# Optimization experiments

Hardware: AMD Instinct MI355X
Metric: run time of the kernel (lower is better)

## Reference

```python
import jax, jax.numpy as jnp
import numpy as np

EPS = 1e-5
GROUPS = 8

def group_norm(x, gamma, beta):
    # x: [B,C,H,W], 8 groups
    B, C, H, W = x.shape
    xg = x.reshape(B, GROUPS, C // GROUPS, H, W)
    mu = jnp.mean(xg, axis=(2, 3, 4), keepdims=True)
    var = jnp.mean((xg - mu) ** 2, axis=(2, 3, 4), keepdims=True)
    xn = ((xg - mu) * jax.lax.rsqrt(var + EPS)).reshape(B, C, H, W)
    return xn * gamma[None, :, None, None] + beta[None, :, None, None]

def setup_inputs() -> dict:
    key = jax.random.key(0)
    ks = jax.random.split(key, 7)
    B, C, H, W = 4, 256, 64, 64
    x = jax.random.normal(ks[0], (B, C, H, W), dtype=jnp.float32)
    gamma = jnp.ones((C,), dtype=jnp.float32)
    beta = jnp.zeros((C,), dtype=jnp.float32)
    s = 1.0 / np.sqrt(C)
    w_qkv = jax.random.normal(ks[1], (3 * C, C), dtype=jnp.float32) * s
    b_qkv = jnp.zeros((3 * C,), dtype=jnp.float32)
    w_proj = jax.random.normal(ks[2], (C, C), dtype=jnp.float32) * s
    b_proj = jnp.zeros((C,), dtype=jnp.float32)
    return {"x": x, "gamma": gamma, "beta": beta, "w_qkv": w_qkv,
            "b_qkv": b_qkv, "w_proj": w_proj, "b_proj": b_proj}

def reference(x, gamma, beta, w_qkv, b_qkv, w_proj, b_proj):
    B, C, H, W = x.shape
    N = H * W
    h = group_norm(x, gamma, beta)
    # 1x1 conv == per-pixel matmul
    qkv = jnp.einsum('bchw,oc->bohw', h, w_qkv) + b_qkv[None, :, None, None]
    q, k, v = jnp.split(qkv, 3, axis=1)  # each [B,C,H,W]
    q = q.reshape(B, C, N).transpose(0, 2, 1)   # [B,N,C]
    k = k.reshape(B, C, N)                      # [B,C,N]
    v = v.reshape(B, C, N).transpose(0, 2, 1)   # [B,N,C]
    attn = jax.nn.softmax(jnp.einsum('bnc,bcm->bnm', q, k) / jnp.sqrt(jnp.float32(C)), axis=-1)
    out = jnp.einsum('bnm,bmc->bnc', attn, v)   # [B,N,C]
    out = out.transpose(0, 2, 1).reshape(B, C, H, W)
    proj = jnp.einsum('bchw,oc->bohw', out, w_proj) + b_proj[None, :, None, None]
    return x + proj
```

## Files before the change

### kernel.cpp

```cpp
#include <hip/hip_runtime.h>
#include <hip/hip_bf16.h>
#include <math.h>

#define B 4
#define C 256
#define G 8
#define N 4096
#define EPSV 1e-5f
#define SCALE 0.0625f

typedef __attribute__((ext_vector_type(8))) short short8;
typedef __attribute__((ext_vector_type(16))) float f32x16;
typedef unsigned short ushort_t;
typedef unsigned int uint_t;

__device__ __forceinline__ ushort_t f2bf(float f) {
    union { float f; uint_t u; } c; c.f = f;
    uint_t u = c.u;
    uint_t r = (u + 0x7FFFu + ((u >> 16) & 1u)) >> 16;
    return (ushort_t)r;
}
__device__ __forceinline__ float bf2f(ushort_t h) {
    union { uint_t u; float f; } c; c.u = ((uint_t)h) << 16;
    return c.f;
}
__device__ __forceinline__ uint_t pack2(float a, float b) {
    return (uint_t)f2bf(a) | ((uint_t)f2bf(b) << 16);
}
__device__ __forceinline__ uint_t cvtpk_bf16(float lo, float hi) {
    uint_t r;
    asm("v_cvt_pk_bf16_f32 %0, %1, %2" : "=v"(r) : "v"(lo), "v"(hi));
    return r;
}
__device__ __forceinline__ void gl_lds16(const void* g, void* l) {
    __builtin_amdgcn_global_load_lds(
        (const __attribute__((address_space(1))) void*)g,
        (__attribute__((address_space(3))) void*)l, 16, 0, 0);
}

__global__ __launch_bounds__(256) void wconv(const float* __restrict__ wq,
        const float* __restrict__ wp, ushort_t* __restrict__ wbf) {
    int idx = blockIdx.x*256 + threadIdx.x;
    #pragma unroll
    for (int p = 0; p < 4; p++) {
        int id = idx + p*16384;
        float4 v = (id < 49152) ? ((const float4*)wq)[id] : ((const float4*)wp)[id - 49152];
        uint2 pk; pk.x = pack2(v.x, v.y); pk.y = pack2(v.z, v.w);
        *(uint2*)&wbf[(size_t)id*4] = pk;
    }
}

__global__ __launch_bounds__(256) void gn_partial(const float* __restrict__ x,
                                                  float* __restrict__ partials) {
    int blk = blockIdx.x;
    int bg = blk >> 3;
    int part = blk & 7;
    const float4* xp4 = (const float4*)(x + (size_t)bg * (32 * N) + (size_t)part * (32 * N / 8));
    float s = 0.f, ss = 0.f;
    for (int i = threadIdx.x; i < 4096; i += 256) {
        float4 v = xp4[i];
        s  += v.x + v.y + v.z + v.w;
        ss += v.x*v.x + v.y*v.y + v.z*v.z + v.w*v.w;
    }
    __shared__ float rs[256], rss[256];
    rs[threadIdx.x] = s; rss[threadIdx.x] = ss;
    __syncthreads();
    for (int off = 128; off > 0; off >>= 1) {
        if (threadIdx.x < off) {
            rs[threadIdx.x]  += rs[threadIdx.x + off];
            rss[threadIdx.x] += rss[threadIdx.x + off];
        }
        __syncthreads();
    }
    if (threadIdx.x == 0) {
        partials[(bg*8 + part)*2]     = rs[0];
        partials[(bg*8 + part)*2 + 1] = rss[0];
    }
}

__global__ void gn_final(const float* __restrict__ partials, float* __restrict__ stats) {
    int t = threadIdx.x;
    if (t < 32) {
        float s = 0.f, ss = 0.f;
        for (int p = 0; p < 8; p++) {
            s  += partials[(t*8 + p)*2];
            ss += partials[(t*8 + p)*2 + 1];
        }
        const float inv = 1.f / 131072.f;
        float mu = s * inv;
        float var = fmaxf(ss * inv - mu*mu, 0.f);
        stats[t*2]     = mu;
        stats[t*2 + 1] = rsqrtf(var + EPSV);
    }
}

__global__ __launch_bounds__(256) void norm_bf16(const float* __restrict__ x,
        const float* __restrict__ gamma, const float* __restrict__ beta,
        const float* __restrict__ stats, ushort_t* __restrict__ hbf) {
    int b = blockIdx.z, c0 = blockIdx.y*64, n0 = blockIdx.x*64;
    int t = threadIdx.x;
    int cq = t >> 4, nq = t & 15;
    ushort_t hv[4][4];
    #pragma unroll
    for (int i = 0; i < 4; i++) {
        int c = c0 + cq*4 + i;
        int g = c >> 5;
        float mu = stats[(b*G+g)*2], rs = stats[(b*G+g)*2+1];
        float ga = gamma[c]*rs;
        float be = beta[c] - mu*ga;
        float4 v = *(const float4*)&x[((size_t)(b*C + c))*N + n0 + nq*4];
        hv[i][0] = f2bf(v.x*ga + be);
        hv[i][1] = f2bf(v.y*ga + be);
        hv[i][2] = f2bf(v.z*ga + be);
        hv[i][3] = f2bf(v.w*ga + be);
    }
    #pragma unroll
    for (int j = 0; j < 4; j++) {
        uint2 pk;
        pk.x = (uint_t)hv[0][j] | ((uint_t)hv[1][j]<<16);
        pk.y = (uint_t)hv[2][j] | ((uint_t)hv[3][j]<<16);
        *(uint2*)&hbf[((size_t)(b*N + n0 + nq*4 + j))*256 + c0 + cq*4] = pk;
    }
}

__global__ __launch_bounds__(256) void qkv_mfma(const ushort_t* __restrict__ hbf,
        const ushort_t* __restrict__ wbf, const float* __restrict__ bias,
        ushort_t* __restrict__ qbf, ushort_t* __restrict__ kimg, ushort_t* __restrict__ vimg) {
    int b = blockIdx.z, o0 = blockIdx.y*128, n0 = blockIdx.x*128;
    int tid = threadIdx.x;
    int w = tid>>6, l = tid&63, l31 = l&31, lh = l>>5;
    __shared__ short Ws[2][8192];
    __shared__ short Hs[2][8192];

    const ushort_t* wb = wbf + (size_t)o0*256;
    const ushort_t* hb = hbf + ((size_t)b*N + n0)*256;

    auto stage = [&](int bb, int c0) {
        #pragma unroll
        for (int q = 0; q < 4; q++) {
            int u0 = (q*4 + w)*64;
            int u  = u0 + l;
            int row = u & 127, ch = u >> 7;
            gl_lds16(wb + (size_t)row*256 + c0 + ch*8, &Ws[bb][u0*8]);
            gl_lds16(hb + (size_t)row*256 + c0 + ch*8, &Hs[bb][u0*8]);
        }
    };

    f32x16 acc[4];
    #pragma unroll
    for (int nf = 0; nf < 4; nf++)
        #pragma unroll
        for (int r = 0; r < 16; r++) acc[nf][r] = 0.f;

    stage(0, 0);
    __syncthreads();
    for (int t = 0; t < 4; t++) {
        int bb = t & 1;
        if (t < 3) stage(bb^1, (t+1)*64);
        short8 af[4];
        #pragma unroll
        for (int s = 0; s < 4; s++)
            af[s] = *(const short8*)&Ws[bb][((2*s+lh)*128 + w*32 + l31)*8];
        #pragma unroll
        for (int nf = 0; nf < 4; nf++) {
            #pragma unroll
            for (int s = 0; s < 4; s++) {
                short8 hf = *(const short8*)&Hs[bb][((2*s+lh)*128 + nf*32 + l31)*8];
                acc[nf] = __builtin_amdgcn_mfma_f32_32x32x16_bf16(af[s], hf, acc[nf], 0, 0, 0);
            }
        }
        __syncthreads();
    }

    int ow = o0 + w*32;
    float bv[16];
    #pragma unroll
    for (int r = 0; r < 16; r++) bv[r] = bias[ow + (r&3) + 8*(r>>2) + 4*lh];

    if (ow < 256) {
        #pragma unroll
        for (int nf = 0; nf < 4; nf++) {
            int n = n0 + nf*32 + l31;
            ushort_t* row = qbf + ((size_t)(b*N + n))*256 + ow;
            #pragma unroll
            for (int rp = 0; rp < 8; rp++) {
                int r0 = rp*2;
                int cl = (r0&3) + 8*(r0>>2) + 4*lh;
                uint_t wd = cvtpk_bf16((acc[nf][r0]+bv[r0])*SCALE, (acc[nf][r0+1]+bv[r0+1])*SCALE);
                *(uint_t*)(row + cl) = wd;
            }
        }
    } else if (ow < 512) {
        int cb = ow - 256;
        #pragma unroll
        for (int nf = 0; nf < 4; nf++) {
            int n = n0 + nf*32 + l31;
            ushort_t* tbase = kimg + (size_t)b*1048576 + (size_t)(n>>5)*8192
                            + (size_t)l31*8 + 4*lh;
            #pragma unroll
            for (int g = 0; g < 4; g++) {
                uint2 pk;
                pk.x = pack2(acc[nf][g*4+0]+bv[g*4+0], acc[nf][g*4+1]+bv[g*4+1]);
                pk.y = pack2(acc[nf][g*4+2]+bv[g*4+2], acc[nf][g*4+3]+bv[g*4+3]);
                *(uint2*)(tbase + (size_t)((cb>>3)+g)*256) = pk;
            }
        }
    } else {
        int cb = ow - 512;
        #pragma unroll
        for (int nf = 0; nf < 4; nf++) {
            int n = n0 + nf*32 + l31;
            ushort_t* tbase = vimg + (size_t)b*1048576 + (size_t)(n>>5)*8192
                            + (size_t)(l31>>3)*2048 + (l31&7);
            #pragma unroll
            for (int r = 0; r < 16; r++) {
                int cl = (r&3) + 8*(r>>2) + 4*lh;
                tbase[(size_t)(cb+cl)*8] = f2bf(acc[nf][r] + bv[r]);
            }
        }
    }
}

__global__ __launch_bounds__(256, 2) void attn_mfma(const ushort_t* __restrict__ qbf,
        const ushort_t* __restrict__ kimg, const ushort_t* __restrict__ vimg,
        ushort_t* __restrict__ part, float* __restrict__ ml) {
    int f = blockIdx.x;
    int comb = f & 15;
    int qt  = f >> 4;
    int b   = comb >> 2;
    int kvq = comb & 3;
    constexpr int NT = 32;
    int w = threadIdx.x >> 6;
    int l = threadIdx.x & 63;
    int l31 = l & 31, lh = l >> 5;

    __shared__ short KV[2][2][8192];

    int qbase = qt*128 + w*32;
    short8 qf[16];
    {
        const ushort_t* qrow = qbf + ((size_t)(b*N + qbase + l31))*256;
        #pragma unroll
        for (int s = 0; s < 16; s++)
            qf[s] = *(const short8*)(qrow + s*16 + lh*8);
    }

    f32x16 ot[8];
    #pragma unroll
    for (int mc = 0; mc < 8; mc++)
        #pragma unroll
        for (int r = 0; r < 16; r++) ot[mc][r] = 0.f;
    float m = -INFINITY, lsum = 0.f;

    const char* kbase = (const char*)kimg + (size_t)b*2097152;
    const char* vbase = (const char*)vimg + (size_t)b*2097152;

    auto stage = [&](int slot, int t) {
        int tile = kvq*32 + t;
        const char* kt = kbase + (size_t)tile*16384;
        const char* vt = vbase + (size_t)tile*16384;
        #pragma unroll
        for (int q = 0; q < 4; q++) {
            int u0 = (w*4 + q)*64;
            gl_lds16(kt + (u0 + l)*16, &KV[slot][0][u0*8]);
            gl_lds16(vt + (u0 + l)*16, &KV[slot][1][u0*8]);
        }
    };

    stage(0, 0);

    for (int t = 0; t < NT; t++) {
        int slot = t & 1;
        __syncthreads();
        if (t+1 < NT) stage(slot^1, t+1);

        f32x16 st0, st1;
        #pragma unroll
        for (int r = 0; r < 16; r++) { st0[r] = 0.f; st1[r] = 0.f; }
        const short* kb_ = &KV[slot][0][0];
        __builtin_amdgcn_s_setprio(1);
        #pragma unroll
        for (int s = 0; s < 8; s++) {
            short8 ka = *(const short8*)(kb_ + ((size_t)((4*s   + lh)*32 + l31))*8);
            short8 kc = *(const short8*)(kb_ + ((size_t)((4*s+2 + lh)*32 + l31))*8);
            st0 = __builtin_amdgcn_mfma_f32_32x32x16_bf16(ka, qf[2*s],   st0, 0, 0, 0);
            st1 = __builtin_amdgcn_mfma_f32_32x32x16_bf16(kc, qf[2*s+1], st1, 0, 0, 0);
        }
        __builtin_amdgcn_s_setprio(0);

        float sv[16];
        #pragma unroll
        for (int r = 0; r < 16; r++) sv[r] = st0[r] + st1[r];
        float pmax = sv[0];
        #pragma unroll
        for (int r = 1; r < 16; r++) pmax = fmaxf(pmax, sv[r]);
        pmax = fmaxf(pmax, __shfl_xor(pmax, 32));
        if (!__all(pmax <= m + 8.0f)) {
            float mn = fmaxf(m, pmax);
            float fac = __expf(m - mn);
            m = mn;
            lsum *= fac;
            #pragma unroll
            for (int mc = 0; mc < 8; mc++)
                #pragma unroll
                for (int r = 0; r < 16; r++) ot[mc][r] *= fac;
        }
        float p[16]; float ls = 0.f;
        #pragma unroll
        for (int r = 0; r < 16; r++) { p[r] = __expf(sv[r] - m); ls += p[r]; }
        ls += __shfl_xor(ls, 32);
        lsum += ls;

        short8 pf0, pf1;
        {
            uint_t x0 = cvtpk_bf16(p[0], p[1]);
            uint_t y0 = cvtpk_bf16(p[4], p[5]);
            uint_t x1 = cvtpk_bf16(p[2], p[3]);
            uint_t y1 = cvtpk_bf16(p[6], p[7]);
            auto r0 = __builtin_amdgcn_permlane32_swap(x0, y0, false, false);
            auto r1 = __builtin_amdgcn_permlane32_swap(x1, y1, false, false);
            union { uint_t u[4]; short8 s8; } u_;
            u_.u[0] = r0[0]; u_.u[1] = r1[0]; u_.u[2] = r0[1]; u_.u[3] = r1[1];
            pf0 = u_.s8;
            uint_t x2 = cvtpk_bf16(p[8],  p[9]);
            uint_t y2 = cvtpk_bf16(p[12], p[13]);
            uint_t x3 = cvtpk_bf16(p[10], p[11]);
            uint_t y3 = cvtpk_bf16(p[14], p[15]);
            auto r2 = __builtin_amdgcn_permlane32_swap(x2, y2, false, false);
            auto r3 = __builtin_amdgcn_permlane32_swap(x3, y3, false, false);
            union { uint_t u[4]; short8 s8; } u2_;
            u2_.u[0] = r2[0]; u2_.u[1] = r3[0]; u2_.u[2] = r2[1]; u2_.u[3] = r3[1];
            pf1 = u2_.s8;
        }

        const short* vb_ = &KV[slot][1][0];
        __builtin_amdgcn_s_setprio(1);
        #pragma unroll
        for (int mc = 0; mc < 8; mc++) {
            short8 v0 = *(const short8*)(vb_ + ((size_t)((lh)*256   + mc*32 + l31))*8);
            short8 v1 = *(const short8*)(vb_ + ((size_t)((2+lh)*256 + mc*32 + l31))*8);
            ot[mc] = __builtin_amdgcn_mfma_f32_32x32x16_bf16(v0, pf0, ot[mc], 0, 0, 0);
            ot[mc] = __builtin_amdgcn_mfma_f32_32x32x16_bf16(v1, pf1, ot[mc], 0, 0, 0);
        }
        __builtin_amdgcn_s_setprio(0);
    }

    float invl = 1.f / lsum;
    ushort_t* pbase = part + (size_t)kvq*4194304 + ((size_t)(b*N + qbase + l31))*256;
    #pragma unroll
    for (int mc = 0; mc < 8; mc++)
        #pragma unroll
        for (int rp = 0; rp < 8; rp++) {
            int r0 = rp*2;
            uint_t wd = cvtpk_bf16(ot[mc][r0]*invl, ot[mc][r0+1]*invl);
            int c0 = (r0 & 3) + 8*(r0 >> 2) + 4*lh + 32*mc;
            *(uint_t*)(pbase + c0) = wd;
        }
    if (l < 32) {
        size_t row = (size_t)kvq*16384 + b*4096 + qbase + l;
        ml[row*2]     = m;
        ml[row*2 + 1] = lsum;
    }
}

template<int NS>
__global__ __launch_bounds__(256) void attn_merge(const ushort_t* __restrict__ part,
        const float* __restrict__ ml, ushort_t* __restrict__ ob) {
    int t = blockIdx.x*256 + threadIdx.x;
    int row = t >> 5;
    int c8 = (t & 31) * 8;
    float mv[NS], lv[NS];
    float M = -INFINITY;
    #pragma unroll
    for (int i = 0; i < NS; i++) {
        mv[i] = ml[((size_t)i*16384 + row)*2];
        lv[i] = ml[((size_t)i*16384 + row)*2 + 1];
        M = fmaxf(M, mv[i]);
    }
    float wv[NS]; float wsum = 0.f;
    #pragma unroll
    for (int i = 0; i < NS; i++) { wv[i] = __expf(mv[i] - M)*lv[i]; wsum += wv[i]; }
    float inv = 1.f / wsum;
    float o[8];
    #pragma unroll
    for (int e = 0; e < 8; e++) o[e] = 0.f;
    #pragma unroll
    for (int i = 0; i < NS; i++) {
        const ushort_t* p = part + (size_t)i*4194304 + (size_t)row*256 + c8;
        float wi = wv[i]*inv;
        #pragma unroll
        for (int e = 0; e < 8; e++) o[e] += wi*bf2f(p[e]);
    }
    uint4 pk;
    pk.x = pack2(o[0], o[1]);
    pk.y = pack2(o[2], o[3]);
    pk.z = pack2(o[4], o[5]);
    pk.w = pack2(o[6], o[7]);
    *(uint4*)(ob + (size_t)row*256 + c8) = pk;
}

__global__ __launch_bounds__(256) void proj_mfma(const ushort_t* __restrict__ obf,
        const ushort_t* __restrict__ wpbf, const float* __restrict__ bp,
        const float* __restrict__ x, float* __restrict__ out) {
    int b = blockIdx.z, o0 = blockIdx.y*128, n0 = blockIdx.x*128;
    int tid = threadIdx.x;
    int w = tid>>6, l = tid&63, l31 = l&31, lh = l>>5;
    __shared__ short Ws[2][8192];
    __shared__ short Hs[2][8192];

    const ushort_t* wb = wpbf + (size_t)o0*256;
    const ushort_t* hb = obf + ((size_t)b*N + n0)*256;

    auto stage = [&](int bb, int c0) {
        #pragma unroll
        for (int q = 0; q < 4; q++) {
            int u0 = (q*4 + w)*64;
            int u  = u0 + l;
            int row = u & 127, ch = u >> 7;
            gl_lds16(wb + (size_t)row*256 + c0 + ch*8, &Ws[bb][u0*8]);
            gl_lds16(hb + (size_t)row*256 + c0 + ch*8, &Hs[bb][u0*8]);
        }
    };

    f32x16 acc[4];
    #pragma unroll
    for (int nf = 0; nf < 4; nf++)
        #pragma unroll
        for (int r = 0; r < 16; r++) acc[nf][r] = 0.f;

    stage(0, 0);
    __syncthreads();
    for (int t = 0; t < 4; t++) {
        int bb = t & 1;
        if (t < 3) stage(bb^1, (t+1)*64);
        short8 af[4];
        #pragma unroll
        for (int s = 0; s < 4; s++)
            af[s] = *(const short8*)&Ws[bb][((2*s+lh)*128 + w*32 + l31)*8];
        #pragma unroll
        for (int nf = 0; nf < 4; nf++) {
            #pragma unroll
            for (int s = 0; s < 4; s++) {
                short8 hf = *(const short8*)&Hs[bb][((2*s+lh)*128 + nf*32 + l31)*8];
                acc[nf] = __builtin_amdgcn_mfma_f32_32x32x16_bf16(af[s], hf, acc[nf], 0, 0, 0);
            }
        }
        __syncthreads();
    }

    int cw = o0 + w*32;
    float bv[16];
    #pragma unroll
    for (int r = 0; r < 16; r++) bv[r] = bp[cw + (r&3) + 8*(r>>2) + 4*lh];

    #pragma unroll
    for (int nf = 0; nf < 4; nf++) {
        int n = n0 + nf*32 + l31;
        #pragma unroll
        for (int r = 0; r < 16; r++) {
            int cl = (r&3) + 8*(r>>2) + 4*lh;
            size_t a = ((size_t)b*C + cw + cl)*N + n;
            out[a] = acc[nf][r] + bv[r] + x[a];
        }
    }
}

extern "C" void kernel_launch(void* const* d_in, const int* in_sizes, int n_in,
                              void* d_out, int out_size, void* d_ws, size_t ws_size,
                              hipStream_t stream) {
    const float* x      = (const float*)d_in[0];
    const float* gamma  = (const float*)d_in[1];
    const float* beta   = (const float*)d_in[2];
    const float* w_qkv  = (const float*)d_in[3];
    const float* b_qkv  = (const float*)d_in[4];
    const float* w_proj = (const float*)d_in[5];
    const float* b_proj = (const float*)d_in[6];
    float* out = (float*)d_out;
    char* wsb  = (char*)d_ws;

    const size_t MB = 1048576;
    ushort_t* qbf  = (ushort_t*)(wsb);
    ushort_t* kimg = (ushort_t*)(wsb + 8*MB);
    ushort_t* vimg = (ushort_t*)(wsb + 16*MB);
    ushort_t* part = (ushort_t*)(wsb + 24*MB);
    ushort_t* hbf  = part;
    float*    ml   = (float*)  (wsb + 56*MB);
    ushort_t* ob   = (ushort_t*)(wsb + 56*MB + 524288);
    float* partials = (float*) (wsb + 64*MB + 524288);
    float* stats    = partials + 512;
    ushort_t* wbf  = (ushort_t*)(wsb + 64*MB + 524288 + 4096);

    wconv<<<dim3(64), dim3(256), 0, stream>>>(w_qkv, w_proj, wbf);
    gn_partial<<<dim3(256), dim3(256), 0, stream>>>(x, partials);
    gn_final<<<dim3(1), dim3(64), 0, stream>>>(partials, stats);
    norm_bf16<<<dim3(64, 4, 4), dim3(256), 0, stream>>>(x, gamma, beta, stats, hbf);
    qkv_mfma<<<dim3(32, 6, 4), dim3(256), 0, stream>>>(hbf, wbf, b_qkv, qbf, kimg, vimg);
    attn_mfma<<<dim3(512), dim3(256), 0, stream>>>(qbf, kimg, vimg, part, ml);
    attn_merge<4><<<dim3(2048), dim3(256), 0, stream>>>(part, ml, ob);
    proj_mfma<<<dim3(32, 2, 4), dim3(256), 0, stream>>>(ob, wbf + 196608, b_proj, x, out);
}
```

Measured before the change: 151.3 us.

## Fuse groupnorm apply into QKV GEMM, merge weight conversion with stats kernel

The separate norm_bf16 pass is removed. The QKV GEMM now loads fp32 x tiles directly, normalizes them, and writes the bf16 result into shared memory, with the next tile's load overlapping the current MFMAs. Weight conversion and the group-norm partial sums share one launch, and the projection GEMM uses a 64-column N tile to double its grid. This saves a full bf16 round-trip of h and two launches, but each QKV block (6 o-tiles) now re-reads x from global memory, and register pressure grows.

```diff
diff --git a/kernel.cpp b/kernel.cpp
--- a/kernel.cpp
+++ b/kernel.cpp
@@ -38,43 +38,43 @@
         (__attribute__((address_space(3))) void*)l, 16, 0, 0);
 }
 
-__global__ __launch_bounds__(256) void wconv(const float* __restrict__ wq,
+__global__ __launch_bounds__(256) void gn_wconv(const float* __restrict__ x,
+        float* __restrict__ partials, const float* __restrict__ wq,
         const float* __restrict__ wp, ushort_t* __restrict__ wbf) {
-    int idx = blockIdx.x*256 + threadIdx.x;
-    #pragma unroll
-    for (int p = 0; p < 4; p++) {
-        int id = idx + p*16384;
-        float4 v = (id < 49152) ? ((const float4*)wq)[id] : ((const float4*)wp)[id - 49152];
-        uint2 pk; pk.x = pack2(v.x, v.y); pk.y = pack2(v.z, v.w);
-        *(uint2*)&wbf[(size_t)id*4] = pk;
-    }
-}
-
-__global__ __launch_bounds__(256) void gn_partial(const float* __restrict__ x,
-                                                  float* __restrict__ partials) {
     int blk = blockIdx.x;
-    int bg = blk >> 3;
-    int part = blk & 7;
-    const float4* xp4 = (const float4*)(x + (size_t)bg * (32 * N) + (size_t)part * (32 * N / 8));
-    float s = 0.f, ss = 0.f;
-    for (int i = threadIdx.x; i < 4096; i += 256) {
-        float4 v = xp4[i];
-        s  += v.x + v.y + v.z + v.w;
-        ss += v.x*v.x + v.y*v.y + v.z*v.z + v.w*v.w;
-    }
-    __shared__ float rs[256], rss[256];
-    rs[threadIdx.x] = s; rss[threadIdx.x] = ss;
-    __syncthreads();
-    for (int off = 128; off > 0; off >>= 1) {
-        if (threadIdx.x < off) {
-            rs[threadIdx.x]  += rs[threadIdx.x + off];
-            rss[threadIdx.x] += rss[threadIdx.x + off];
-        }
+    if (blk < 256) {
+        int bg = blk >> 3;
+        int part = blk & 7;
+        const float4* xp4 = (const float4*)(x + (size_t)bg * (32 * N) + (size_t)part * (32 * N / 8));
+        float s = 0.f, ss = 0.f;
+        for (int i = threadIdx.x; i < 4096; i += 256) {
+            float4 v = xp4[i];
+            s  += v.x + v.y + v.z + v.w;
+            ss += v.x*v.x + v.y*v.y + v.z*v.z + v.w*v.w;
+        }
+        __shared__ float rs[256], rss[256];
+        rs[threadIdx.x] = s; rss[threadIdx.x] = ss;
         __syncthreads();
-    }
-    if (threadIdx.x == 0) {
-        partials[(bg*8 + part)*2]     = rs[0];
-        partials[(bg*8 + part)*2 + 1] = rss[0];
+        for (int off = 128; off > 0; off >>= 1) {
+            if (threadIdx.x < off) {
+                rs[threadIdx.x]  += rs[threadIdx.x + off];
+                rss[threadIdx.x] += rss[threadIdx.x + off];
+            }
+            __syncthreads();
+        }
+        if (threadIdx.x == 0) {
+            partials[(bg*8 + part)*2]     = rs[0];
+            partials[(bg*8 + part)*2 + 1] = rss[0];
+        }
+    } else {
+        int idx = (blk - 256)*256 + threadIdx.x;
+        #pragma unroll
+        for (int p = 0; p < 4; p++) {
+            int id = idx + p*16384;
+            float4 v = (id < 49152) ? ((const float4*)wq)[id] : ((const float4*)wp)[id - 49152];
+            uint2 pk; pk.x = pack2(v.x, v.y); pk.y = pack2(v.z, v.w);
+            *(uint2*)&wbf[(size_t)id*4] = pk;
+        }
     }
 }
 
@@ -94,57 +94,63 @@
     }
 }
 
-__global__ __launch_bounds__(256) void norm_bf16(const float* __restrict__ x,
-        const float* __restrict__ gamma, const float* __restrict__ beta,
-        const float* __restrict__ stats, ushort_t* __restrict__ hbf) {
-    int b = blockIdx.z, c0 = blockIdx.y*64, n0 = blockIdx.x*64;
-    int t = threadIdx.x;
-    int cq = t >> 4, nq = t & 15;
-    ushort_t hv[4][4];
-    #pragma unroll
-    for (int i = 0; i < 4; i++) {
-        int c = c0 + cq*4 + i;
-        int g = c >> 5;
-        float mu = stats[(b*G+g)*2], rs = stats[(b*G+g)*2+1];
-        float ga = gamma[c]*rs;
-        float be = beta[c] - mu*ga;
-        float4 v = *(const float4*)&x[((size_t)(b*C + c))*N + n0 + nq*4];
-        hv[i][0] = f2bf(v.x*ga + be);
-        hv[i][1] = f2bf(v.y*ga + be);
-        hv[i][2] = f2bf(v.z*ga + be);
-        hv[i][3] = f2bf(v.w*ga + be);
-    }
-    #pragma unroll
-    for (int j = 0; j < 4; j++) {
-        uint2 pk;
-        pk.x = (uint_t)hv[0][j] | ((uint_t)hv[1][j]<<16);
-        pk.y = (uint_t)hv[2][j] | ((uint_t)hv[3][j]<<16);
-        *(uint2*)&hbf[((size_t)(b*N + n0 + nq*4 + j))*256 + c0 + cq*4] = pk;
-    }
-}
-
-__global__ __launch_bounds__(256) void qkv_mfma(const ushort_t* __restrict__ hbf,
-        const ushort_t* __restrict__ wbf, const float* __restrict__ bias,
+__global__ __launch_bounds__(256) void qkv_fused(const float* __restrict__ x,
+        const ushort_t* __restrict__ wbf, const float* __restrict__ gamma,
+        const float* __restrict__ beta, const float* __restrict__ stats,
+        const float* __restrict__ bias,
         ushort_t* __restrict__ qbf, ushort_t* __restrict__ kimg, ushort_t* __restrict__ vimg) {
     int b = blockIdx.z, o0 = blockIdx.y*128, n0 = blockIdx.x*128;
     int tid = threadIdx.x;
     int w = tid>>6, l = tid&63, l31 = l&31, lh = l>>5;
+    int cg = tid >> 5;
+    int nq = tid & 31;
     __shared__ short Ws[2][8192];
     __shared__ short Hs[2][8192];
 
     const ushort_t* wb = wbf + (size_t)o0*256;
-    const ushort_t* hb = hbf + ((size_t)b*N + n0)*256;
-
-    auto stage = [&](int bb, int c0) {
+
+    auto stageW = [&](int bb, int c0) {
         #pragma unroll
         for (int q = 0; q < 4; q++) {
             int u0 = (q*4 + w)*64;
             int u  = u0 + l;
             int row = u & 127, ch = u >> 7;
             gl_lds16(wb + (size_t)row*256 + c0 + ch*8, &Ws[bb][u0*8]);
-            gl_lds16(hb + (size_t)row*256 + c0 + ch*8, &Hs[bb][u0*8]);
         }
     };
+    auto loadX = [&](int c0, float4* xv) {
+        const float* xb = x + ((size_t)b*C + c0 + cg*8)*N + n0 + nq*4;
+        #pragma unroll
+        for (int e = 0; e < 8; e++)
+            xv[e] = *(const float4*)(xb + (size_t)e*N);
+    };
+    auto writeH = [&](int bb, int c0, const float4* xv) {
+        int cbase = c0 + cg*8;
+        int g = cbase >> 5;
+        float mu = stats[(b*G+g)*2], rs = stats[(b*G+g)*2+1];
+        float ga[8], be[8];
+        #pragma unroll
+        for (int e = 0; e < 8; e++) {
+            float gm = gamma[cbase+e];
+            ga[e] = gm*rs;
+            be[e] = beta[cbase+e] - mu*ga[e];
+        }
+        #pragma unroll
+        for (int j = 0; j < 4; j++) {
+            float h[8];
+            #pragma unroll
+            for (int e = 0; e < 8; e++) {
+                float vx = (j==0) ? xv[e].x : (j==1) ? xv[e].y : (j==2) ? xv[e].z : xv[e].w;
+                h[e] = vx*ga[e] + be[e];
+            }
+            uint4 pk;
+            pk.x = pack2(h[0], h[1]);
+            pk.y = pack2(h[2], h[3]);
+            pk.z = pack2(h[4], h[5]);
+            pk.w = pack2(h[6], h[7]);
+            *(uint4*)&Hs[bb][(size_t)(cg*128 + nq*4 + j)*8] = pk;
+        }
+    };
 
     f32x16 acc[4];
     #pragma unroll
@@ -152,11 +158,15 @@
         #pragma unroll
         for (int r = 0; r < 16; r++) acc[nf][r] = 0.f;
 
-    stage(0, 0);
+    float4 xv[8];
+    loadX(0, xv);
+    stageW(0, 0);
+    writeH(0, 0, xv);
     __syncthreads();
+
     for (int t = 0; t < 4; t++) {
         int bb = t & 1;
-        if (t < 3) stage(bb^1, (t+1)*64);
+        if (t < 3) { stageW(bb^1, (t+1)*64); loadX((t+1)*64, xv); }
         short8 af[4];
         #pragma unroll
         for (int s = 0; s < 4; s++)
@@ -169,6 +179,7 @@
                 acc[nf] = __builtin_amdgcn_mfma_f32_32x32x16_bf16(af[s], hf, acc[nf], 0, 0, 0);
             }
         }
+        if (t < 3) writeH(bb^1, (t+1)*64, xv);
         __syncthreads();
     }
 
@@ -402,11 +413,11 @@
 __global__ __launch_bounds__(256) void proj_mfma(const ushort_t* __restrict__ obf,
         const ushort_t* __restrict__ wpbf, const float* __restrict__ bp,
         const float* __restrict__ x, float* __restrict__ out) {
-    int b = blockIdx.z, o0 = blockIdx.y*128, n0 = blockIdx.x*128;
+    int b = blockIdx.z, o0 = blockIdx.y*128, n0 = blockIdx.x*64;
     int tid = threadIdx.x;
     int w = tid>>6, l = tid&63, l31 = l&31, lh = l>>5;
     __shared__ short Ws[2][8192];
-    __shared__ short Hs[2][8192];
+    __shared__ short Hs[2][4096];
 
     const ushort_t* wb = wpbf + (size_t)o0*256;
     const ushort_t* hb = obf + ((size_t)b*N + n0)*256;
@@ -418,13 +429,19 @@
             int u  = u0 + l;
             int row = u & 127, ch = u >> 7;
             gl_lds16(wb + (size_t)row*256 + c0 + ch*8, &Ws[bb][u0*8]);
+        }
+        #pragma unroll
+        for (int q = 0; q < 2; q++) {
+            int u0 = (q*4 + w)*64;
+            int u  = u0 + l;
+            int row = u & 63, ch = u >> 6;
             gl_lds16(hb + (size_t)row*256 + c0 + ch*8, &Hs[bb][u0*8]);
         }
     };
 
-    f32x16 acc[4];
-    #pragma unroll
-    for (int nf = 0; nf < 4; nf++)
+    f32x16 acc[2];
+    #pragma unroll
+    for (int nf = 0; nf < 2; nf++)
         #pragma unroll
         for (int r = 0; r < 16; r++) acc[nf][r] = 0.f;
 
@@ -438,10 +455,10 @@
         for (int s = 0; s < 4; s++)
             af[s] = *(const short8*)&Ws[bb][((2*s+lh)*128 + w*32 + l31)*8];
         #pragma unroll
-        for (int nf = 0; nf < 4; nf++) {
+        for (int nf = 0; nf < 2; nf++) {
             #pragma unroll
             for (int s = 0; s < 4; s++) {
-                short8 hf = *(const short8*)&Hs[bb][((2*s+lh)*128 + nf*32 + l31)*8];
+                short8 hf = *(const short8*)&Hs[bb][((2*s+lh)*64 + nf*32 + l31)*8];
                 acc[nf] = __builtin_amdgcn_mfma_f32_32x32x16_bf16(af[s], hf, acc[nf], 0, 0, 0);
             }
         }
@@ -454,7 +471,7 @@
     for (int r = 0; r < 16; r++) bv[r] = bp[cw + (r&3) + 8*(r>>2) + 4*lh];
 
     #pragma unroll
-    for (int nf = 0; nf < 4; nf++) {
+    for (int nf = 0; nf < 2; nf++) {
         int n = n0 + nf*32 + l31;
         #pragma unroll
         for (int r = 0; r < 16; r++) {
@@ -483,19 +500,16 @@
     ushort_t* kimg = (ushort_t*)(wsb + 8*MB);
     ushort_t* vimg = (ushort_t*)(wsb + 16*MB);
     ushort_t* part = (ushort_t*)(wsb + 24*MB);
-    ushort_t* hbf  = part;
     float*    ml   = (float*)  (wsb + 56*MB);
     ushort_t* ob   = (ushort_t*)(wsb + 56*MB + 524288);
     float* partials = (float*) (wsb + 64*MB + 524288);
     float* stats    = partials + 512;
     ushort_t* wbf  = (ushort_t*)(wsb + 64*MB + 524288 + 4096);
 
-    wconv<<<dim3(64), dim3(256), 0, stream>>>(w_qkv, w_proj, wbf);
-    gn_partial<<<dim3(256), dim3(256), 0, stream>>>(x, partials);
+    gn_wconv<<<dim3(320), dim3(256), 0, stream>>>(x, partials, w_qkv, w_proj, wbf);
     gn_final<<<dim3(1), dim3(64), 0, stream>>>(partials, stats);
-    norm_bf16<<<dim3(64, 4, 4), dim3(256), 0, stream>>>(x, gamma, beta, stats, hbf);
-    qkv_mfma<<<dim3(32, 6, 4), dim3(256), 0, stream>>>(hbf, wbf, b_qkv, qbf, kimg, vimg);
+    qkv_fused<<<dim3(32, 6, 4), dim3(256), 0, stream>>>(x, wbf, gamma, beta, stats, b_qkv, qbf, kimg, vimg);
     attn_mfma<<<dim3(512), dim3(256), 0, stream>>>(qbf, kimg, vimg, part, ml);
     attn_merge<4><<<dim3(2048), dim3(256), 0, stream>>>(part, ml, ob);
-    proj_mfma<<<dim3(32, 2, 4), dim3(256), 0, stream>>>(ob, wbf + 196608, b_proj, x, out);
-}
+    proj_mfma<<<dim3(64, 2, 4), dim3(256), 0, stream>>>(ob, wbf + 196608, b_proj, x, out);
+}
```

After: 137.2 us. 1.1x faster.
